# Kernel optimization log

Hardware: AMD Instinct MI355X
Metric: run time of the kernel (lower is better)

The kernel has to match this reference:

```python
import jax, jax.numpy as jnp
import numpy as np

N_NODES = 50000
N_FEAT = 63          # nodeChannels C = N_FEAT + 1 = 64
N_EDGES = 800000
N_LABELS = 10000
BATCH = 4
N_LAYERS = 5
C = N_FEAT + 1


def setup_inputs() -> dict:
    key = jax.random.key(0)
    ks = jax.random.split(key, 16)
    s = 0.05  # small init scale for numerical sanity
    return {
        "cov": jax.random.normal(ks[0], (BATCH, N_LABELS), jnp.float32),
        "nodes": jax.random.normal(ks[1], (N_NODES, N_FEAT), jnp.float32),
        "edges": jax.random.randint(ks[2], (2, N_EDGES), 0, N_NODES, jnp.int64 if jax.config.jax_enable_x64 else jnp.int32),
        "count2label": jnp.arange(N_LABELS, dtype=jnp.int32),
        "ggc_weight": jax.random.normal(ks[3], (N_LAYERS, C, C), jnp.float32) * s,
        "gru_w_ih": jax.random.normal(ks[4], (3 * C, C), jnp.float32) * s,
        "gru_w_hh": jax.random.normal(ks[5], (3 * C, C), jnp.float32) * s,
        "gru_b_ih": jax.random.normal(ks[6], (3 * C,), jnp.float32) * s,
        "gru_b_hh": jax.random.normal(ks[7], (3 * C,), jnp.float32) * s,
        "ai_w": jax.random.normal(ks[8], (2 * C, 2 * C), jnp.float32) * s,
        "ai_b": jax.random.normal(ks[9], (2 * C,), jnp.float32) * s,
        "aj_w": jax.random.normal(ks[10], (2 * C, 2 * C), jnp.float32) * s,
        "aj_b": jax.random.normal(ks[11], (2 * C,), jnp.float32) * s,
        "mlp_w": jax.random.normal(ks[12], (256, 2 * C), jnp.float32) * s,
        "mlp_b": jax.random.normal(ks[13], (256,), jnp.float32) * s,
        "critic_w": jax.random.normal(ks[14], (1, 256), jnp.float32) * s,
        "critic_b": jax.random.normal(ks[15], (1,), jnp.float32) * s,
    }


def _gru_cell(m, h, w_ih, w_hh, b_ih, b_hh):
    # torch GRUCell, gate order r, z, n
    gx = m @ w_ih.T + b_ih   # [..., 3C]
    gh = h @ w_hh.T + b_hh
    c = h.shape[-1]
    xr, xz, xn = gx[..., :c], gx[..., c:2 * c], gx[..., 2 * c:]
    hr, hz, hn = gh[..., :c], gh[..., c:2 * c], gh[..., 2 * c:]
    r = jax.nn.sigmoid(xr + hr)
    z = jax.nn.sigmoid(xz + hz)
    n = jnp.tanh(xn + r * hn)
    return (1.0 - z) * n + z * h


def reference(cov, nodes, edges, count2label, ggc_weight,
              gru_w_ih, gru_w_hh, gru_b_ih, gru_b_hh,
              ai_w, ai_b, aj_w, aj_b, mlp_w, mlp_b, critic_w, critic_b):
    n, f = nodes.shape
    b = cov.shape[0]
    # scatter coverage into per-graph node channel: covInGraph[count2label] = cov
    cov_in_graph = jnp.zeros((b, n), cov.dtype).at[:, count2label].set(cov)
    # batched node input [B, N, C]; batched graph = B identical copies w/ offset edges
    x0 = jnp.concatenate(
        [jnp.broadcast_to(nodes, (b, n, f)), cov_in_graph[..., None]], axis=-1)
    src, dst = edges[0], edges[1]

    def scatter_add(mb):  # [N, C] -> [N, C]: sum messages from source at target
        return jax.ops.segment_sum(mb[src], dst, num_segments=n)

    x = x0
    for i in range(ggc_weight.shape[0]):
        m = x @ ggc_weight[i]                     # dense per-layer matmul [B,N,C]
        agg = jax.vmap(scatter_add)(m)            # edge scatter-add propagate
        x = _gru_cell(agg, x, gru_w_ih, gru_w_hh, gru_b_ih, gru_b_hh)

    # attention gate: sigmoid(Wi cat) * relu(Wj cat), cat = [x, x0]
    cat = jnp.concatenate([x, x0], axis=-1)       # [B, N, 2C]
    att = jax.nn.sigmoid(cat @ ai_w.T + ai_b) * jax.nn.relu(cat @ aj_w.T + aj_b)
    pooled = jax.nn.relu(att.sum(axis=1))         # global_add_pool -> [B, 2C]
    state = jax.nn.relu(pooled @ mlp_w.T + mlp_b) # graphmlp
    return state @ critic_w.T + critic_b          # critic value [B, 1]
```

## Files before the change

kernel.cpp:

```cpp
#include <hip/hip_runtime.h>
#include <math.h>

#define NN 50000
#define NF 63
#define NE 800000
#define NL 10000
#define NB 4
#define NLAY 5
#define BN (NB*NN)
#define NTILES (BN/64)
#define SCAN_NBLK ((NN+255)/256)
#define HIST_NBLK ((NE+255)/256)

using f32x4  = __attribute__((ext_vector_type(4))) float;
using f32x2  = __attribute__((ext_vector_type(2))) float;
using bf16x8 = __attribute__((ext_vector_type(8))) __bf16;

__device__ __forceinline__ float frcp(float x){ return __builtin_amdgcn_rcpf(x); }
__device__ __forceinline__ float sigm(float v){ return frcp(1.f + __expf(-v)); }
__device__ __forceinline__ float tanh_f(float v){ return fmaf(-2.f, frcp(__expf(2.f*v) + 1.f), 1.f); }

__device__ __forceinline__ ushort f2bf(float f){
    uint u = __builtin_bit_cast(uint, f);
    u += 0x7fffu + ((u >> 16) & 1u);
    return (ushort)(u >> 16);
}
__device__ __forceinline__ float bf_lo(uint v){ return __builtin_bit_cast(float, v << 16); }
__device__ __forceinline__ float bfu(ushort v){ return __builtin_bit_cast(float, ((uint)v) << 16); }

__device__ __forceinline__ uchar f2fp8(float v){
    int enc = __builtin_amdgcn_cvt_pk_fp8_f32(v, v, 0, false);
    return (uchar)(enc & 0xff);
}

__device__ __forceinline__ bf16x8 ldfrag(const ushort* p){
    uint4 v = *(const uint4*)p;
    return __builtin_bit_cast(bf16x8, v);
}
__device__ __forceinline__ f32x4 MFMA(bf16x8 a, bf16x8 b, f32x4 c){
    return __builtin_amdgcn_mfma_f32_16x16x32_bf16(a, b, c, 0, 0, 0);
}

__global__ void k_setup(const int* __restrict__ edges, int* __restrict__ cnt,
                        const float* __restrict__ wih, const float* __restrict__ whh,
                        const float* __restrict__ aiw, const float* __restrict__ ajw,
                        const float* __restrict__ ggc,
                        ushort* __restrict__ whhb, ushort* __restrict__ aiwb,
                        ushort* __restrict__ ajwb, ushort* __restrict__ wfb){
    int bid = blockIdx.x;
    if (bid < HIST_NBLK){
        int e = bid*256 + threadIdx.x;
        if (e < NE) atomicAdd(&cnt[edges[NE + e]], 1);
        return;
    }
    int i = (bid - HIST_NBLK)*256 + threadIdx.x;
    if (i < 12288)        whhb[i]        = f2bf(whh[i]);
    else if (i < 28672)   aiwb[i-12288]  = f2bf(aiw[i-12288]);
    else if (i < 45056)   ajwb[i-28672]  = f2bf(ajw[i-28672]);
    else if (i < 106496){
        int t = i - 45056;
        int lay = t / 12288;
        int rem = t % 12288;
        int n = rem >> 6, k = rem & 63;
        const float* W  = ggc + lay*4096 + k*64;
        const float* wr = wih + n*64;
        float s = 0.f;
        #pragma unroll 8
        for (int c = 0; c < 64; ++c) s = fmaf(W[c], wr[c], s);
        wfb[t] = f2bf(s);
    }
}

__global__ void k_scan1(const int* __restrict__ cnt, int* __restrict__ tmp, int* __restrict__ bsum){
    __shared__ int sh[256];
    int tx = threadIdx.x, i = blockIdx.x*256 + tx;
    int v = (i < NN) ? cnt[i] : 0;
    sh[tx] = v; __syncthreads();
    for (int off = 1; off < 256; off <<= 1){
        int u = (tx >= off) ? sh[tx-off] : 0;
        __syncthreads();
        sh[tx] += u;
        __syncthreads();
    }
    int incl = sh[tx];
    if (i < NN) tmp[i] = incl - v;
    if (tx == 255) bsum[blockIdx.x] = incl;
}

__global__ void k_scan2(const int* __restrict__ bsum, int* __restrict__ boff){
    __shared__ int sh[256];
    int tx = threadIdx.x;
    int v = (tx < SCAN_NBLK) ? bsum[tx] : 0;
    sh[tx] = v; __syncthreads();
    for (int off = 1; off < 256; off <<= 1){
        int u = (tx >= off) ? sh[tx-off] : 0;
        __syncthreads();
        sh[tx] += u;
        __syncthreads();
    }
    boff[tx] = sh[tx] - v;
}

__global__ void k_scan3(const int* __restrict__ tmp, const int* __restrict__ boff,
                        int* __restrict__ row_start, int* __restrict__ cursor){
    int i = blockIdx.x*256 + threadIdx.x;
    if (i < NN){
        int rs = tmp[i] + boff[blockIdx.x];
        row_start[i] = rs;
        cursor[i] = rs;
    }
    if (i == 0) row_start[NN] = NE;
}

__global__ void k_fillcsr(const int* __restrict__ edges, int* __restrict__ cursor, int* __restrict__ csr_src){
    int e = blockIdx.x*256 + threadIdx.x;
    if (e < NE){
        int d = edges[NE + e];
        int pos = atomicAdd(&cursor[d], 1);
        csr_src[pos] = edges[e];
    }
}

__global__ void k_x0(const float* __restrict__ nodes, ushort* __restrict__ x0I,
                     uchar* __restrict__ x0F){
    int f = blockIdx.x*256 + threadIdx.x;
    int row = f >> 4, c4 = f & 15;
    int n = row % NN, b = row / NN;
    float v[4];
    #pragma unroll
    for (int i = 0; i < 4; ++i){
        int c = c4*4 + i;
        v[i] = (c < NF) ? nodes[(size_t)n*NF + c] : 0.f;
    }
    uint2 pk;
    pk.x = (uint)f2bf(v[0]) | ((uint)f2bf(v[1]) << 16);
    pk.y = (uint)f2bf(v[2]) | ((uint)f2bf(v[3]) << 16);
    *(uint2*)(x0I + ((size_t)n*4 + b)*64 + c4*4) = pk;
    if (b == 0){
        uint q = 0;
        q = (uint)__builtin_amdgcn_cvt_pk_fp8_f32(v[0], v[1], (int)q, false);
        q = (uint)__builtin_amdgcn_cvt_pk_fp8_f32(v[2], v[3], (int)q, true);
        *(uint*)(x0F + (size_t)n*64 + c4*4) = q;
    }
}

__global__ void k_cov(const float* __restrict__ cov, const int* __restrict__ c2l,
                      ushort* __restrict__ x0I, ushort* __restrict__ covB){
    int i = blockIdx.x*256 + threadIdx.x;
    if (i < NB*NL){
        int b = i / NL, j = i % NL;
        int nd = c2l[j];
        ushort vb = f2bf(cov[i]);
        x0I[((size_t)nd*4 + b)*64 + 63] = vb;
        covB[(size_t)nd*4 + b] = vb;
    }
}

template<bool LI>
__device__ __forceinline__ void gather0q(const uchar* __restrict__ x0F,
                                         const ushort* __restrict__ covB,
                                         const int* __restrict__ row_start,
                                         const int* __restrict__ csr_src,
                                         const int* sIdx, int estart,
                                         int d0, int l, ushort* __restrict__ sAgg,
                                         int rbase){
    const int qn = l >> 4, t = l & 15;
    const uint off = (uint)(t*4);
    const int d = d0 + qn;
    const int e0 = row_start[d], e1 = row_start[d+1];
    f32x2 a01 = (f32x2){0.f,0.f}, a23 = (f32x2){0.f,0.f};
    float c = 0.f;
    int e = e0;
    for (; e + 8 <= e1; e += 8){
        int s[8];
        #pragma unroll
        for (int j = 0; j < 8; ++j) s[j] = LI ? sIdx[e + j - estart] : csr_src[e + j];
        uint v[8];
        #pragma unroll
        for (int j = 0; j < 8; ++j) v[j] = *(const uint*)(x0F + (size_t)s[j]*64 + off);
        #pragma unroll
        for (int j = 0; j < 8; ++j){
            a01 += __builtin_amdgcn_cvt_pk_f32_fp8(v[j], false);
            a23 += __builtin_amdgcn_cvt_pk_f32_fp8(v[j], true);
        }
        if (t < 4){
            #pragma unroll
            for (int j = 0; j < 8; ++j) c += bf_lo((uint)covB[(size_t)s[j]*4 + t]);
        }
    }
    if (e < e1){
        #pragma unroll
        for (int j = 0; j < 8; ++j){
            int ee = e + j; bool ok = ee < e1; if (!ok) ee = e1 - 1;
            int s = LI ? sIdx[ee - estart] : csr_src[ee];
            uint v = *(const uint*)(x0F + (size_t)s*64 + off);
            if (!ok) v = 0u;
            a01 += __builtin_amdgcn_cvt_pk_f32_fp8(v, false);
            a23 += __builtin_amdgcn_cvt_pk_f32_fp8(v, true);
            if (t < 4){
                float cv = bf_lo((uint)covB[(size_t)s*4 + t]);
                c += ok ? cv : 0.f;
            }
        }
    }
    uint2 pk;
    pk.x = (uint)f2bf(a01.x) | ((uint)f2bf(a01.y) << 16);
    pk.y = (uint)f2bf(a23.x) | ((uint)f2bf(a23.y) << 16);
    #pragma unroll
    for (int b = 0; b < 4; ++b){
        float cb = __shfl(c, (l & 48) | b);
        uint2 o = pk;
        if (t == 15) o.y = (o.y & 0xffffu) | ((uint)f2bf(cb) << 16);
        *(uint2*)(&sAgg[(size_t)(rbase + qn*4 + b)*72 + t*4]) = o;
    }
}

template<bool LI>
__device__ __forceinline__ void gather4q(const uchar* __restrict__ xF,
                                         const int* __restrict__ row_start,
                                         const int* __restrict__ csr_src,
                                         const int* sIdx, int estart,
                                         int d0, int l, ushort* __restrict__ sAgg,
                                         int rbase){
    const int qn = l >> 4;
    const int t  = l & 15;
    const uint off = (uint)(t*16);
    const int d = d0 + qn;
    const int e0 = row_start[d], e1 = row_start[d+1];
    f32x2 ac[8];
    #pragma unroll
    for (int k = 0; k < 8; ++k) ac[k] = (f32x2){0.f,0.f};

    int e = e0;
    for (; e + 8 <= e1; e += 8){
        int s[8];
        #pragma unroll
        for (int j = 0; j < 8; ++j) s[j] = LI ? sIdx[e + j - estart] : csr_src[e + j];
        uint4 v[8];
        #pragma unroll
        for (int j = 0; j < 8; ++j) v[j] = *(const uint4*)(xF + (size_t)s[j]*256 + off);
        #pragma unroll
        for (int j = 0; j < 8; ++j){
            ac[0] += __builtin_amdgcn_cvt_pk_f32_fp8(v[j].x, false);
            ac[1] += __builtin_amdgcn_cvt_pk_f32_fp8(v[j].x, true);
            ac[2] += __builtin_amdgcn_cvt_pk_f32_fp8(v[j].y, false);
            ac[3] += __builtin_amdgcn_cvt_pk_f32_fp8(v[j].y, true);
            ac[4] += __builtin_amdgcn_cvt_pk_f32_fp8(v[j].z, false);
            ac[5] += __builtin_amdgcn_cvt_pk_f32_fp8(v[j].z, true);
            ac[6] += __builtin_amdgcn_cvt_pk_f32_fp8(v[j].w, false);
            ac[7] += __builtin_amdgcn_cvt_pk_f32_fp8(v[j].w, true);
        }
    }
    if (e < e1){
        #pragma unroll
        for (int j = 0; j < 8; ++j){
            int ee = e + j; bool ok = ee < e1; if (!ok) ee = e1 - 1;
            int s = LI ? sIdx[ee - estart] : csr_src[ee];
            uint4 v = *(const uint4*)(xF + (size_t)s*256 + off);
            if (!ok) v = (uint4){0u,0u,0u,0u};
            ac[0] += __builtin_amdgcn_cvt_pk_f32_fp8(v.x, false);
            ac[1] += __builtin_amdgcn_cvt_pk_f32_fp8(v.x, true);
            ac[2] += __builtin_amdgcn_cvt_pk_f32_fp8(v.y, false);
            ac[3] += __builtin_amdgcn_cvt_pk_f32_fp8(v.y, true);
            ac[4] += __builtin_amdgcn_cvt_pk_f32_fp8(v.z, false);
            ac[5] += __builtin_amdgcn_cvt_pk_f32_fp8(v.z, true);
            ac[6] += __builtin_amdgcn_cvt_pk_f32_fp8(v.w, false);
            ac[7] += __builtin_amdgcn_cvt_pk_f32_fp8(v.w, true);
        }
    }

    const int row = rbase + qn*4 + (t >> 2);
    const int c0  = (t & 3)*16;
    uint4 o0, o1;
    o0.x = (uint)f2bf(ac[0].x) | ((uint)f2bf(ac[0].y) << 16);
    o0.y = (uint)f2bf(ac[1].x) | ((uint)f2bf(ac[1].y) << 16);
    o0.z = (uint)f2bf(ac[2].x) | ((uint)f2bf(ac[2].y) << 16);
    o0.w = (uint)f2bf(ac[3].x) | ((uint)f2bf(ac[3].y) << 16);
    o1.x = (uint)f2bf(ac[4].x) | ((uint)f2bf(ac[4].y) << 16);
    o1.y = (uint)f2bf(ac[5].x) | ((uint)f2bf(ac[5].y) << 16);
    o1.z = (uint)f2bf(ac[6].x) | ((uint)f2bf(ac[6].y) << 16);
    o1.w = (uint)f2bf(ac[7].x) | ((uint)f2bf(ac[7].y) << 16);
    *(uint4*)(&sAgg[(size_t)row*72 + c0])     = o0;
    *(uint4*)(&sAgg[(size_t)row*72 + c0 + 8]) = o1;
}

__device__ __forceinline__ void gru_core(const ushort* sAgg, const ushort* sX,
                                         const ushort* __restrict__ wfb, const ushort* __restrict__ whhb,
                                         const float* __restrict__ bih, const float* __restrict__ bhh,
                                         int li, int q, int n0, float xv[4][4]){
    f32x4 Cr[4], Cz[4], Cxn[4], Chn[4];
    #pragma unroll
    for (int m = 0; m < 4; ++m){
        Cr[m]=(f32x4){0.f,0.f,0.f,0.f}; Cz[m]=(f32x4){0.f,0.f,0.f,0.f};
        Cxn[m]=(f32x4){0.f,0.f,0.f,0.f}; Chn[m]=(f32x4){0.f,0.f,0.f,0.f};
    }
    __builtin_amdgcn_s_setprio(1);
    #pragma unroll
    for (int ks = 0; ks < 4; ++ks){
        const ushort* wb = (ks < 2) ? wfb : whhb;
        const ushort* sT = (ks < 2) ? sAgg : sX;
        const int kb = (ks & 1)*32;
        bf16x8 Br = ldfrag(wb + (size_t)(n0 + li)*64 + kb + q*8);
        bf16x8 Bz = ldfrag(wb + (size_t)(64 + n0 + li)*64 + kb + q*8);
        bf16x8 Bn = ldfrag(wb + (size_t)(128 + n0 + li)*64 + kb + q*8);
        #pragma unroll
        for (int m = 0; m < 4; ++m){
            bf16x8 A = ldfrag(&sT[(m*16 + li)*72 + kb + q*8]);
            Cr[m] = MFMA(A, Br, Cr[m]);
            Cz[m] = MFMA(A, Bz, Cz[m]);
            if (ks < 2) Cxn[m] = MFMA(A, Bn, Cxn[m]);
            else        Chn[m] = MFMA(A, Bn, Chn[m]);
        }
    }
    __builtin_amdgcn_s_setprio(0);
    const int c = n0 + li;
    const float br_ = bih[c]     + bhh[c];
    const float bz_ = bih[64+c]  + bhh[64+c];
    const float bn_ = bih[128+c];
    const float bh_ = bhh[128+c];
    #pragma unroll
    for (int m = 0; m < 4; ++m){
        #pragma unroll
        for (int rg = 0; rg < 4; ++rg){
            int rl = m*16 + q*4 + rg;
            float r = sigm(Cr[m][rg] + br_);
            float z = sigm(Cz[m][rg] + bz_);
            float nng = tanh_f(Cxn[m][rg] + bn_ + r*(Chn[m][rg] + bh_));
            xv[m][rg] = (1.f - z)*nng + z*bfu(sX[rl*72 + c]);
        }
    }
}

__global__ __launch_bounds__(256) void k_gru0f(const uchar* __restrict__ x0F,
                                               const ushort* __restrict__ covB,
                                               const int* __restrict__ row_start,
                                               const int* __restrict__ csr_src,
                                               const ushort* __restrict__ x0I,
                                               const ushort* __restrict__ wfb, const ushort* __restrict__ whhb,
                                               const float* __restrict__ bih, const float* __restrict__ bhh,
                                               ushort* __restrict__ xout, uchar* __restrict__ xFout){
    __shared__ __align__(16) ushort sAgg[64*72];
    __shared__ __align__(16) ushort sX[64*72];
    __shared__ int sIdx[1024];
    const int tx = threadIdx.x;
    const int l  = tx & 63, li = l & 15, q = l >> 4;
    const int w  = __builtin_amdgcn_readfirstlane(tx >> 6);
    const int R0 = blockIdx.x*64;
    const int n0 = blockIdx.x*16;
    const int estart = row_start[n0], eend = row_start[n0 + 16];
    const int ecnt = eend - estart;

    #pragma unroll
    for (int it = 0; it < 2; ++it){
        int idx = it*256 + tx, r = idx >> 3, g = idx & 7;
        *(uint4*)(&sX[r*72 + g*8]) = *(const uint4*)(x0I + (size_t)(R0 + r)*64 + g*8);
    }
    for (int k = tx; k < ecnt && k < 1024; k += 256) sIdx[k] = csr_src[estart + k];
    __syncthreads();

    if (ecnt <= 1024) gather0q<true >(x0F, covB, row_start, csr_src, sIdx, estart, n0 + w*4, l, sAgg, w*16);
    else              gather0q<false>(x0F, covB, row_start, csr_src, sIdx, estart, n0 + w*4, l, sAgg, w*16);
    __syncthreads();

    float xv[4][4];
    gru_core(sAgg, sX, wfb, whhb, bih, bhh, li, q, 16*w, xv);

    const int c = 16*w + li;
    #pragma unroll
    for (int m = 0; m < 4; ++m)
        #pragma unroll
        for (int rg = 0; rg < 4; ++rg){
            size_t ro = (size_t)(R0 + m*16 + q*4 + rg)*64 + c;
            xout[ro]  = f2bf(xv[m][rg]);
            xFout[ro] = f2fp8(xv[m][rg]);
        }
}

__global__ __launch_bounds__(256) void k_gruFf(const uchar* __restrict__ xFin,
                                               const int* __restrict__ row_start,
                                               const int* __restrict__ csr_src,
                                               const ushort* __restrict__ xsrc,
                                               const ushort* __restrict__ wfb, const ushort* __restrict__ whhb,
                                               const float* __restrict__ bih, const float* __restrict__ bhh,
                                               ushort* __restrict__ xout, uchar* __restrict__ xFout){
    __shared__ __align__(16) ushort sAgg[64*72];
    __shared__ __align__(16) ushort sX[64*72];
    __shared__ int sIdx[1024];
    const int tx = threadIdx.x;
    const int l  = tx & 63, li = l & 15, q = l >> 4;
    const int w  = __builtin_amdgcn_readfirstlane(tx >> 6);
    const int R0 = blockIdx.x*64;
    const int n0 = blockIdx.x*16;
    const int estart = row_start[n0], eend = row_start[n0 + 16];
    const int ecnt = eend - estart;

    #pragma unroll
    for (int it = 0; it < 2; ++it){
        int idx = it*256 + tx, r = idx >> 3, g = idx & 7;
        *(uint4*)(&sX[r*72 + g*8]) = *(const uint4*)(xsrc + (size_t)(R0 + r)*64 + g*8);
    }
    for (int k = tx; k < ecnt && k < 1024; k += 256) sIdx[k] = csr_src[estart + k];
    __syncthreads();

    if (ecnt <= 1024) gather4q<true >(xFin, row_start, csr_src, sIdx, estart, n0 + w*4, l, sAgg, w*16);
    else              gather4q<false>(xFin, row_start, csr_src, sIdx, estart, n0 + w*4, l, sAgg, w*16);
    __syncthreads();

    float xv[4][4];
    gru_core(sAgg, sX, wfb, whhb, bih, bhh, li, q, 16*w, xv);

    const int c = 16*w + li;
    #pragma unroll
    for (int m = 0; m < 4; ++m)
        #pragma unroll
        for (int rg = 0; rg < 4; ++rg){
            size_t ro = (size_t)(R0 + m*16 + q*4 + rg)*64 + c;
            xout[ro]  = f2bf(xv[m][rg]);
            xFout[ro] = f2fp8(xv[m][rg]);
        }
}

__global__ __launch_bounds__(256) void k_gruLf(const uchar* __restrict__ xFin,
                                               const int* __restrict__ row_start,
                                               const int* __restrict__ csr_src,
                                               const ushort* __restrict__ xsrc,
                                               const ushort* __restrict__ wfb, const ushort* __restrict__ whhb,
                                               const float* __restrict__ bih, const float* __restrict__ bhh,
                                               const ushort* __restrict__ x0I,
                                               const ushort* __restrict__ aiwb, const float* __restrict__ aib,
                                               const ushort* __restrict__ ajwb, const float* __restrict__ ajb,
                                               float* __restrict__ pooled16){
    __shared__ __align__(16) ushort sAgg[64*72];
    __shared__ __align__(16) ushort sX[64*72];
    __shared__ int sIdx[1024];
    const int tx = threadIdx.x;
    const int l  = tx & 63, li = l & 15, q = l >> 4;
    const int w  = __builtin_amdgcn_readfirstlane(tx >> 6);
    const int R0 = blockIdx.x*64;
    const int n0 = blockIdx.x*16;
    const int estart = row_start[n0], eend = row_start[n0 + 16];
    const int ecnt = eend - estart;

    #pragma unroll
    for (int it = 0; it < 2; ++it){
        int idx = it*256 + tx, r = idx >> 3, g = idx & 7;
        *(uint4*)(&sX[r*72 + g*8]) = *(const uint4*)(xsrc + (size_t)(R0 + r)*64 + g*8);
    }
    for (int k = tx; k < ecnt && k < 1024; k += 256) sIdx[k] = csr_src[estart + k];
    __syncthreads();

    if (ecnt <= 1024) gather4q<true >(xFin, row_start, csr_src, sIdx, estart, n0 + w*4, l, sAgg, w*16);
    else              gather4q<false>(xFin, row_start, csr_src, sIdx, estart, n0 + w*4, l, sAgg, w*16);
    __syncthreads();

    float xv[4][4];
    gru_core(sAgg, sX, wfb, whhb, bih, bhh, li, q, 16*w, xv);
    __syncthreads();

    const int c = 16*w + li;
    #pragma unroll
    for (int m = 0; m < 4; ++m)
        #pragma unroll
        for (int rg = 0; rg < 4; ++rg)
            sAgg[(m*16 + q*4 + rg)*72 + c] = f2bf(xv[m][rg]);
    #pragma unroll
    for (int it = 0; it < 2; ++it){
        int idx = it*256 + tx, r = idx >> 3, g = idx & 7;
        *(uint4*)(&sX[r*72 + g*8]) = *(const uint4*)(x0I + (size_t)(R0 + r)*64 + g*8);
    }
    __syncthreads();

    f32x4 Ai[2][4], Aj[2][4];
    #pragma unroll
    for (int t = 0; t < 2; ++t)
        #pragma unroll
        for (int m = 0; m < 4; ++m){ Ai[t][m]=(f32x4){0.f,0.f,0.f,0.f}; Aj[t][m]=(f32x4){0.f,0.f,0.f,0.f}; }

    const int nb0 = 32*w;
    __builtin_amdgcn_s_setprio(1);
    #pragma unroll
    for (int ks = 0; ks < 4; ++ks){
        const ushort* sT = (ks < 2) ? sAgg : sX;
        const int kb = (ks & 1)*32;
        bf16x8 Bi[2], Bj[2];
        #pragma unroll
        for (int t = 0; t < 2; ++t){
            Bi[t] = ldfrag(aiwb + (size_t)(nb0 + 16*t + li)*128 + ks*32 + q*8);
            Bj[t] = ldfrag(ajwb + (size_t)(nb0 + 16*t + li)*128 + ks*32 + q*8);
        }
        #pragma unroll
        for (int m = 0; m < 4; ++m){
            bf16x8 A = ldfrag(&sT[(m*16 + li)*72 + kb + q*8]);
            #pragma unroll
            for (int t = 0; t < 2; ++t){
                Ai[t][m] = MFMA(A, Bi[t], Ai[t][m]);
                Aj[t][m] = MFMA(A, Bj[t], Aj[t][m]);
            }
        }
    }
    __builtin_amdgcn_s_setprio(0);

    float* pb = pooled16 + (size_t)(blockIdx.x & 15)*512;
    #pragma unroll
    for (int t = 0; t < 2; ++t){
        int cc = nb0 + 16*t + li;
        float bia = aib[cc], bja = ajb[cc];
        float vs[4] = {0.f, 0.f, 0.f, 0.f};
        #pragma unroll
        for (int m = 0; m < 4; ++m){
            #pragma unroll
            for (int rg = 0; rg < 4; ++rg){
                float s = sigm(Ai[t][m][rg] + bia);
                float a = Aj[t][m][rg] + bja;
                a = a > 0.f ? a : 0.f;
                vs[rg] += s*a;
            }
        }
        #pragma unroll
        for (int b = 0; b < 4; ++b){
            vs[b] += __shfl_xor(vs[b], 16);
            vs[b] += __shfl_xor(vs[b], 32);
        }
        if (l < 16){
            #pragma unroll
            for (int b = 0; b < 4; ++b) atomicAdd(&pb[b*128 + nb0 + 16*t + l], vs[b]);
        }
    }
}

__global__ void k_final(const float* __restrict__ pooled16, const float* __restrict__ mw,
                        const float* __restrict__ mb, const float* __restrict__ cw,
                        const float* __restrict__ cb, float* __restrict__ out){
    __shared__ float red[256];
    int t = threadIdx.x;
    int b = blockIdx.x;
    float acc = mb[t];
    #pragma unroll 4
    for (int k = 0; k < 128; ++k){
        float p = 0.f;
        #pragma unroll
        for (int kb = 0; kb < 16; ++kb) p += pooled16[kb*512 + b*128 + k];
        p = p > 0.f ? p : 0.f;
        acc = fmaf(p, mw[t*128 + k], acc);
    }
    float st = acc > 0.f ? acc : 0.f;
    red[t] = st * cw[t];
    __syncthreads();
    for (int off = 128; off > 0; off >>= 1){
        if (t < off) red[t] += red[t + off];
        __syncthreads();
    }
    if (t == 0) out[b] = red[0] + cb[0];
}

extern "C" void kernel_launch(void* const* d_in, const int* in_sizes, int n_in,
                              void* d_out, int out_size, void* d_ws, size_t ws_size,
                              hipStream_t stream) {
    const float* cov   = (const float*)d_in[0];
    const float* nodes = (const float*)d_in[1];
    const int*   edges = (const int*)d_in[2];
    const int*   c2l   = (const int*)d_in[3];
    const float* ggc   = (const float*)d_in[4];
    const float* wih   = (const float*)d_in[5];
    const float* whh   = (const float*)d_in[6];
    const float* bih   = (const float*)d_in[7];
    const float* bhh   = (const float*)d_in[8];
    const float* aiw   = (const float*)d_in[9];
    const float* aib   = (const float*)d_in[10];
    const float* ajw   = (const float*)d_in[11];
    const float* ajb   = (const float*)d_in[12];
    const float* mlpw  = (const float*)d_in[13];
    const float* mlpb  = (const float*)d_in[14];
    const float* cw    = (const float*)d_in[15];
    const float* cb    = (const float*)d_in[16];
    float* out = (float*)d_out;

    const size_t XSZ = (size_t)BN * 64;
    float* ws = (float*)d_ws;
    float* pooled16 = ws;
    ushort* xS    = (ushort*)(pooled16 + 8192);
    ushort* x0I   = xS + XSZ;
    ushort* aggx  = x0I + XSZ;
    ushort* covB  = aggx + XSZ;
    ushort* whhb  = covB + (size_t)NN*4;
    ushort* aiwb  = whhb + 12288;
    ushort* ajwb  = aiwb + 16384;
    ushort* wfb   = ajwb + 16384;
    uchar* xF     = (uchar*)(wfb + 61440);
    uchar* x0F    = xF + XSZ;
    int* cnt       = (int*)(x0F + (size_t)NN*64);
    int* tmp       = cnt + NN;
    int* bsum      = tmp + NN;
    int* boff      = bsum + 256;
    int* row_start = boff + 256;
    int* cursor    = row_start + (NN + 1);
    int* csr_src   = cursor + NN;

    hipMemsetAsync(cnt, 0, (size_t)NN*sizeof(int), stream);
    hipMemsetAsync(pooled16, 0, 8192*sizeof(float), stream);
    hipMemsetAsync(covB, 0, (size_t)NN*4*sizeof(ushort), stream);

    k_setup<<<HIST_NBLK + 416, 256, 0, stream>>>(edges, cnt, wih, whh, aiw, ajw, ggc,
                                                 whhb, aiwb, ajwb, wfb);
    k_scan1<<<SCAN_NBLK, 256, 0, stream>>>(cnt, tmp, bsum);
    k_scan2<<<1, 256, 0, stream>>>(bsum, boff);
    k_scan3<<<SCAN_NBLK, 256, 0, stream>>>(tmp, boff, row_start, cursor);
    k_fillcsr<<<(NE + 255)/256, 256, 0, stream>>>(edges, cursor, csr_src);

    k_x0<<<(BN*16)/256, 256, 0, stream>>>(nodes, x0I, x0F);
    k_cov<<<(NB*NL + 255)/256, 256, 0, stream>>>(cov, c2l, x0I, covB);

    uchar* xFbuf[2] = { xF, (uchar*)aggx };

    for (int i = 0; i < NLAY; ++i){
        const ushort* wf = wfb + (size_t)i*12288;
        if (i == 0){
            k_gru0f<<<NTILES, 256, 0, stream>>>(x0F, covB, row_start, csr_src, x0I,
                                                wf, whhb, bih, bhh, xS, xFbuf[0]);
        } else if (i < NLAY - 1){
            k_gruFf<<<NTILES, 256, 0, stream>>>(xFbuf[(i+1)&1], row_start, csr_src, xS,
                                                wf, whhb, bih, bhh, xS, xFbuf[i&1]);
        } else {
            k_gruLf<<<NTILES, 256, 0, stream>>>(xFbuf[(i+1)&1], row_start, csr_src, xS,
                                                wf, whhb, bih, bhh,
                                                x0I, aiwb, aib, ajwb, ajb, pooled16);
        }
    }

    k_final<<<NB, 256, 0, stream>>>(pooled16, mlpw, mlpb, cw, cb, out);
    (void)in_sizes; (void)n_in; (void)out_size; (void)ws_size;
}
```

Measured before the change: 568.8 us.

## Fuse setup kernels, drop LDS index staging, unroll gathers, coalesce state stores

Folds the x0 conversion into the setup launch and the coverage scatter into the first scan launch, which removes two kernel launches. Removes the shared-memory staging of CSR indices so the gathers read csr_src directly, and raises the gather unroll from 8 to 16 for more loads in flight. GRU output is now staged through LDS and written as coalesced 16-byte bf16 and fp8 stores instead of scattered scalar stores. Launch bounds request 4 blocks per CU; the wider unroll raises register pressure.

Measured after the change: 490.1 us. -13.8%, faster.

```diff
diff --git a/kernel.cpp b/kernel.cpp
--- a/kernel.cpp
+++ b/kernel.cpp
@@ -11,6 +11,8 @@
 #define NTILES (BN/64)
 #define SCAN_NBLK ((NN+255)/256)
 #define HIST_NBLK ((NE+255)/256)
+#define X0_NBLK ((BN*16)/256)
+#define COV_NBLK ((NB*NL+255)/256)
 
 using f32x4  = __attribute__((ext_vector_type(4))) float;
 using f32x2  = __attribute__((ext_vector_type(2))) float;
@@ -26,12 +28,8 @@
     return (ushort)(u >> 16);
 }
 __device__ __forceinline__ float bf_lo(uint v){ return __builtin_bit_cast(float, v << 16); }
+__device__ __forceinline__ float bf_hi(uint v){ return __builtin_bit_cast(float, v & 0xffff0000u); }
 __device__ __forceinline__ float bfu(ushort v){ return __builtin_bit_cast(float, ((uint)v) << 16); }
-
-__device__ __forceinline__ uchar f2fp8(float v){
-    int enc = __builtin_amdgcn_cvt_pk_fp8_f32(v, v, 0, false);
-    return (uchar)(enc & 0xff);
-}
 
 __device__ __forceinline__ bf16x8 ldfrag(const ushort* p){
     uint4 v = *(const uint4*)p;
@@ -46,32 +44,69 @@
                         const float* __restrict__ aiw, const float* __restrict__ ajw,
                         const float* __restrict__ ggc,
                         ushort* __restrict__ whhb, ushort* __restrict__ aiwb,
-                        ushort* __restrict__ ajwb, ushort* __restrict__ wfb){
+                        ushort* __restrict__ ajwb, ushort* __restrict__ wfb,
+                        const float* __restrict__ nodes, ushort* __restrict__ x0I,
+                        uchar* __restrict__ x0F){
     int bid = blockIdx.x;
     if (bid < HIST_NBLK){
         int e = bid*256 + threadIdx.x;
         if (e < NE) atomicAdd(&cnt[edges[NE + e]], 1);
         return;
     }
-    int i = (bid - HIST_NBLK)*256 + threadIdx.x;
-    if (i < 12288)        whhb[i]        = f2bf(whh[i]);
-    else if (i < 28672)   aiwb[i-12288]  = f2bf(aiw[i-12288]);
-    else if (i < 45056)   ajwb[i-28672]  = f2bf(ajw[i-28672]);
-    else if (i < 106496){
-        int t = i - 45056;
-        int lay = t / 12288;
-        int rem = t % 12288;
-        int n = rem >> 6, k = rem & 63;
-        const float* W  = ggc + lay*4096 + k*64;
-        const float* wr = wih + n*64;
-        float s = 0.f;
-        #pragma unroll 8
-        for (int c = 0; c < 64; ++c) s = fmaf(W[c], wr[c], s);
-        wfb[t] = f2bf(s);
-    }
-}
-
-__global__ void k_scan1(const int* __restrict__ cnt, int* __restrict__ tmp, int* __restrict__ bsum){
+    if (bid < HIST_NBLK + 416){
+        int i = (bid - HIST_NBLK)*256 + threadIdx.x;
+        if (i < 12288)        whhb[i]        = f2bf(whh[i]);
+        else if (i < 28672)   aiwb[i-12288]  = f2bf(aiw[i-12288]);
+        else if (i < 45056)   ajwb[i-28672]  = f2bf(ajw[i-28672]);
+        else if (i < 106496){
+            int t = i - 45056;
+            int lay = t / 12288;
+            int rem = t % 12288;
+            int n = rem >> 6, k = rem & 63;
+            const float* W  = ggc + lay*4096 + k*64;
+            const float* wr = wih + n*64;
+            float s = 0.f;
+            #pragma unroll 8
+            for (int c = 0; c < 64; ++c) s = fmaf(W[c], wr[c], s);
+            wfb[t] = f2bf(s);
+        }
+        return;
+    }
+    int f = (bid - HIST_NBLK - 416)*256 + threadIdx.x;
+    int row = f >> 4, c4 = f & 15;
+    int n = row % NN, b = row / NN;
+    float v[4];
+    #pragma unroll
+    for (int i = 0; i < 4; ++i){
+        int c = c4*4 + i;
+        v[i] = (c < NF) ? nodes[(size_t)n*NF + c] : 0.f;
+    }
+    uint2 pk;
+    pk.x = (uint)f2bf(v[0]) | ((uint)f2bf(v[1]) << 16);
+    pk.y = (uint)f2bf(v[2]) | ((uint)f2bf(v[3]) << 16);
+    *(uint2*)(x0I + ((size_t)n*4 + b)*64 + c4*4) = pk;
+    if (b == 0){
+        uint q = 0;
+        q = (uint)__builtin_amdgcn_cvt_pk_fp8_f32(v[0], v[1], (int)q, false);
+        q = (uint)__builtin_amdgcn_cvt_pk_fp8_f32(v[2], v[3], (int)q, true);
+        *(uint*)(x0F + (size_t)n*64 + c4*4) = q;
+    }
+}
+
+__global__ void k_scan1(const int* __restrict__ cnt, int* __restrict__ tmp, int* __restrict__ bsum,
+                        const float* __restrict__ cov, const int* __restrict__ c2l,
+                        ushort* __restrict__ x0I, ushort* __restrict__ covB){
+    if (blockIdx.x >= SCAN_NBLK){
+        int i = (blockIdx.x - SCAN_NBLK)*256 + threadIdx.x;
+        if (i < NB*NL){
+            int b = i / NL, j = i % NL;
+            int nd = c2l[j];
+            ushort vb = f2bf(cov[i]);
+            x0I[((size_t)nd*4 + b)*64 + 63] = vb;
+            covB[(size_t)nd*4 + b] = vb;
+        }
+        return;
+    }
     __shared__ int sh[256];
     int tx = threadIdx.x, i = blockIdx.x*256 + tx;
     int v = (i < NN) ? cnt[i] : 0;
@@ -121,47 +156,10 @@
     }
 }
 
-__global__ void k_x0(const float* __restrict__ nodes, ushort* __restrict__ x0I,
-                     uchar* __restrict__ x0F){
-    int f = blockIdx.x*256 + threadIdx.x;
-    int row = f >> 4, c4 = f & 15;
-    int n = row % NN, b = row / NN;
-    float v[4];
-    #pragma unroll
-    for (int i = 0; i < 4; ++i){
-        int c = c4*4 + i;
-        v[i] = (c < NF) ? nodes[(size_t)n*NF + c] : 0.f;
-    }
-    uint2 pk;
-    pk.x = (uint)f2bf(v[0]) | ((uint)f2bf(v[1]) << 16);
-    pk.y = (uint)f2bf(v[2]) | ((uint)f2bf(v[3]) << 16);
-    *(uint2*)(x0I + ((size_t)n*4 + b)*64 + c4*4) = pk;
-    if (b == 0){
-        uint q = 0;
-        q = (uint)__builtin_amdgcn_cvt_pk_fp8_f32(v[0], v[1], (int)q, false);
-        q = (uint)__builtin_amdgcn_cvt_pk_fp8_f32(v[2], v[3], (int)q, true);
-        *(uint*)(x0F + (size_t)n*64 + c4*4) = q;
-    }
-}
-
-__global__ void k_cov(const float* __restrict__ cov, const int* __restrict__ c2l,
-                      ushort* __restrict__ x0I, ushort* __restrict__ covB){
-    int i = blockIdx.x*256 + threadIdx.x;
-    if (i < NB*NL){
-        int b = i / NL, j = i % NL;
-        int nd = c2l[j];
-        ushort vb = f2bf(cov[i]);
-        x0I[((size_t)nd*4 + b)*64 + 63] = vb;
-        covB[(size_t)nd*4 + b] = vb;
-    }
-}
-
-template<bool LI>
 __device__ __forceinline__ void gather0q(const uchar* __restrict__ x0F,
                                          const ushort* __restrict__ covB,
                                          const int* __restrict__ row_start,
                                          const int* __restrict__ csr_src,
-                                         const int* sIdx, int estart,
                                          int d0, int l, ushort* __restrict__ sAgg,
                                          int rbase){
     const int qn = l >> 4, t = l & 15;
@@ -171,35 +169,43 @@
     f32x2 a01 = (f32x2){0.f,0.f}, a23 = (f32x2){0.f,0.f};
     float c = 0.f;
     int e = e0;
-    for (; e + 8 <= e1; e += 8){
-        int s[8];
-        #pragma unroll
-        for (int j = 0; j < 8; ++j) s[j] = LI ? sIdx[e + j - estart] : csr_src[e + j];
-        uint v[8];
-        #pragma unroll
-        for (int j = 0; j < 8; ++j) v[j] = *(const uint*)(x0F + (size_t)s[j]*64 + off);
-        #pragma unroll
-        for (int j = 0; j < 8; ++j){
+    for (; e + 16 <= e1; e += 16){
+        int s[16];
+        #pragma unroll
+        for (int j = 0; j < 16; ++j) s[j] = csr_src[e + j];
+        uint v[16];
+        #pragma unroll
+        for (int j = 0; j < 16; ++j) v[j] = *(const uint*)(x0F + (size_t)s[j]*64 + off);
+        #pragma unroll
+        for (int j = 0; j < 16; ++j){
             a01 += __builtin_amdgcn_cvt_pk_f32_fp8(v[j], false);
             a23 += __builtin_amdgcn_cvt_pk_f32_fp8(v[j], true);
         }
         if (t < 4){
             #pragma unroll
-            for (int j = 0; j < 8; ++j) c += bf_lo((uint)covB[(size_t)s[j]*4 + t]);
+            for (int j = 0; j < 16; ++j) c += bf_lo((uint)covB[(size_t)s[j]*4 + t]);
         }
     }
     if (e < e1){
-        #pragma unroll
-        for (int j = 0; j < 8; ++j){
-            int ee = e + j; bool ok = ee < e1; if (!ok) ee = e1 - 1;
-            int s = LI ? sIdx[ee - estart] : csr_src[ee];
-            uint v = *(const uint*)(x0F + (size_t)s*64 + off);
-            if (!ok) v = 0u;
-            a01 += __builtin_amdgcn_cvt_pk_f32_fp8(v, false);
-            a23 += __builtin_amdgcn_cvt_pk_f32_fp8(v, true);
-            if (t < 4){
-                float cv = bf_lo((uint)covB[(size_t)s*4 + t]);
-                c += ok ? cv : 0.f;
+        int s[16];
+        #pragma unroll
+        for (int j = 0; j < 16; ++j){ int ee = e + j; if (ee >= e1) ee = e1 - 1; s[j] = csr_src[ee]; }
+        uint v[16];
+        #pragma unroll
+        for (int j = 0; j < 16; ++j){
+            v[j] = *(const uint*)(x0F + (size_t)s[j]*64 + off);
+            if (e + j >= e1) v[j] = 0u;
+        }
+        #pragma unroll
+        for (int j = 0; j < 16; ++j){
+            a01 += __builtin_amdgcn_cvt_pk_f32_fp8(v[j], false);
+            a23 += __builtin_amdgcn_cvt_pk_f32_fp8(v[j], true);
+        }
+        if (t < 4){
+            #pragma unroll
+            for (int j = 0; j < 16; ++j){
+                float cv = bf_lo((uint)covB[(size_t)s[j]*4 + t]);
+                c += (e + j < e1) ? cv : 0.f;
             }
         }
     }
@@ -215,11 +221,9 @@
     }
 }
 
-template<bool LI>
 __device__ __forceinline__ void gather4q(const uchar* __restrict__ xF,
                                          const int* __restrict__ row_start,
                                          const int* __restrict__ csr_src,
-                                         const int* sIdx, int estart,
                                          int d0, int l, ushort* __restrict__ sAgg,
                                          int rbase){
     const int qn = l >> 4;
@@ -232,15 +236,15 @@
     for (int k = 0; k < 8; ++k) ac[k] = (f32x2){0.f,0.f};
 
     int e = e0;
-    for (; e + 8 <= e1; e += 8){
-        int s[8];
-        #pragma unroll
-        for (int j = 0; j < 8; ++j) s[j] = LI ? sIdx[e + j - estart] : csr_src[e + j];
-        uint4 v[8];
-        #pragma unroll
-        for (int j = 0; j < 8; ++j) v[j] = *(const uint4*)(xF + (size_t)s[j]*256 + off);
-        #pragma unroll
-        for (int j = 0; j < 8; ++j){
+    for (; e + 16 <= e1; e += 16){
+        int s[16];
+        #pragma unroll
+        for (int j = 0; j < 16; ++j) s[j] = csr_src[e + j];
+        uint4 v[16];
+        #pragma unroll
+        for (int j = 0; j < 16; ++j) v[j] = *(const uint4*)(xF + (size_t)s[j]*256 + off);
+        #pragma unroll
+        for (int j = 0; j < 16; ++j){
             ac[0] += __builtin_amdgcn_cvt_pk_f32_fp8(v[j].x, false);
             ac[1] += __builtin_amdgcn_cvt_pk_f32_fp8(v[j].x, true);
             ac[2] += __builtin_amdgcn_cvt_pk_f32_fp8(v[j].y, false);
@@ -252,20 +256,25 @@
         }
     }
     if (e < e1){
-        #pragma unroll
-        for (int j = 0; j < 8; ++j){
-            int ee = e + j; bool ok = ee < e1; if (!ok) ee = e1 - 1;
-            int s = LI ? sIdx[ee - estart] : csr_src[ee];
-            uint4 v = *(const uint4*)(xF + (size_t)s*256 + off);
-            if (!ok) v = (uint4){0u,0u,0u,0u};
-            ac[0] += __builtin_amdgcn_cvt_pk_f32_fp8(v.x, false);
-            ac[1] += __builtin_amdgcn_cvt_pk_f32_fp8(v.x, true);
-            ac[2] += __builtin_amdgcn_cvt_pk_f32_fp8(v.y, false);
-            ac[3] += __builtin_amdgcn_cvt_pk_f32_fp8(v.y, true);
-            ac[4] += __builtin_amdgcn_cvt_pk_f32_fp8(v.z, false);
-            ac[5] += __builtin_amdgcn_cvt_pk_f32_fp8(v.z, true);
-            ac[6] += __builtin_amdgcn_cvt_pk_f32_fp8(v.w, false);
-            ac[7] += __builtin_amdgcn_cvt_pk_f32_fp8(v.w, true);
+        int s[16];
+        #pragma unroll
+        for (int j = 0; j < 16; ++j){ int ee = e + j; if (ee >= e1) ee = e1 - 1; s[j] = csr_src[ee]; }
+        uint4 v[16];
+        #pragma unroll
+        for (int j = 0; j < 16; ++j){
+            v[j] = *(const uint4*)(xF + (size_t)s[j]*256 + off);
+            if (e + j >= e1) v[j] = (uint4){0u,0u,0u,0u};
+        }
+        #pragma unroll
+        for (int j = 0; j < 16; ++j){
+            ac[0] += __builtin_amdgcn_cvt_pk_f32_fp8(v[j].x, false);
+            ac[1] += __builtin_amdgcn_cvt_pk_f32_fp8(v[j].x, true);
+            ac[2] += __builtin_amdgcn_cvt_pk_f32_fp8(v[j].y, false);
+            ac[3] += __builtin_amdgcn_cvt_pk_f32_fp8(v[j].y, true);
+            ac[4] += __builtin_amdgcn_cvt_pk_f32_fp8(v[j].z, false);
+            ac[5] += __builtin_amdgcn_cvt_pk_f32_fp8(v[j].z, true);
+            ac[6] += __builtin_amdgcn_cvt_pk_f32_fp8(v[j].w, false);
+            ac[7] += __builtin_amdgcn_cvt_pk_f32_fp8(v[j].w, true);
         }
     }
 
@@ -331,7 +340,45 @@
     }
 }
 
-__global__ __launch_bounds__(256) void k_gru0f(const uchar* __restrict__ x0F,
+__device__ __forceinline__ void store_state(ushort* sAgg, int tx, int w, int li, int q,
+                                            const float xv[4][4], int R0,
+                                            ushort* __restrict__ xout, uchar* __restrict__ xFout){
+    __syncthreads();
+    const int c = 16*w + li;
+    #pragma unroll
+    for (int m = 0; m < 4; ++m)
+        #pragma unroll
+        for (int rg = 0; rg < 4; ++rg)
+            sAgg[(m*16 + q*4 + rg)*72 + c] = f2bf(xv[m][rg]);
+    __syncthreads();
+    #pragma unroll
+    for (int it = 0; it < 2; ++it){
+        int idx = it*256 + tx, r = idx >> 3, g = idx & 7;
+        *(uint4*)(xout + (size_t)(R0 + r)*64 + g*8) = *(const uint4*)(&sAgg[r*72 + g*8]);
+    }
+    {
+        int r = tx >> 2, g = tx & 3;
+        const ushort* src = &sAgg[r*72 + g*16];
+        uint4 a = *(const uint4*)src;
+        uint4 b = *(const uint4*)(src + 8);
+        uint4 o; uint qd;
+        qd = (uint)__builtin_amdgcn_cvt_pk_fp8_f32(bf_lo(a.x), bf_hi(a.x), 0, false);
+        qd = (uint)__builtin_amdgcn_cvt_pk_fp8_f32(bf_lo(a.y), bf_hi(a.y), (int)qd, true);
+        o.x = qd;
+        qd = (uint)__builtin_amdgcn_cvt_pk_fp8_f32(bf_lo(a.z), bf_hi(a.z), 0, false);
+        qd = (uint)__builtin_amdgcn_cvt_pk_fp8_f32(bf_lo(a.w), bf_hi(a.w), (int)qd, true);
+        o.y = qd;
+        qd = (uint)__builtin_amdgcn_cvt_pk_fp8_f32(bf_lo(b.x), bf_hi(b.x), 0, false);
+        qd = (uint)__builtin_amdgcn_cvt_pk_fp8_f32(bf_lo(b.y), bf_hi(b.y), (int)qd, true);
+        o.z = qd;
+        qd = (uint)__builtin_amdgcn_cvt_pk_fp8_f32(bf_lo(b.z), bf_hi(b.z), 0, false);
+        qd = (uint)__builtin_amdgcn_cvt_pk_fp8_f32(bf_lo(b.w), bf_hi(b.w), (int)qd, true);
+        o.w = qd;
+        *(uint4*)(xFout + (size_t)(R0 + r)*64 + g*16) = o;
+    }
+}
+
+__global__ __launch_bounds__(256, 4) void k_gru0f(const uchar* __restrict__ x0F,
                                                const ushort* __restrict__ covB,
                                                const int* __restrict__ row_start,
                                                const int* __restrict__ csr_src,
@@ -341,42 +388,25 @@
                                                ushort* __restrict__ xout, uchar* __restrict__ xFout){
     __shared__ __align__(16) ushort sAgg[64*72];
     __shared__ __align__(16) ushort sX[64*72];
-    __shared__ int sIdx[1024];
     const int tx = threadIdx.x;
     const int l  = tx & 63, li = l & 15, q = l >> 4;
     const int w  = __builtin_amdgcn_readfirstlane(tx >> 6);
     const int R0 = blockIdx.x*64;
-    const int n0 = blockIdx.x*16;
-    const int estart = row_start[n0], eend = row_start[n0 + 16];
-    const int ecnt = eend - estart;
 
     #pragma unroll
     for (int it = 0; it < 2; ++it){
         int idx = it*256 + tx, r = idx >> 3, g = idx & 7;
         *(uint4*)(&sX[r*72 + g*8]) = *(const uint4*)(x0I + (size_t)(R0 + r)*64 + g*8);
     }
-    for (int k = tx; k < ecnt && k < 1024; k += 256) sIdx[k] = csr_src[estart + k];
-    __syncthreads();
-
-    if (ecnt <= 1024) gather0q<true >(x0F, covB, row_start, csr_src, sIdx, estart, n0 + w*4, l, sAgg, w*16);
-    else              gather0q<false>(x0F, covB, row_start, csr_src, sIdx, estart, n0 + w*4, l, sAgg, w*16);
+    gather0q(x0F, covB, row_start, csr_src, blockIdx.x*16 + w*4, l, sAgg, w*16);
     __syncthreads();
 
     float xv[4][4];
     gru_core(sAgg, sX, wfb, whhb, bih, bhh, li, q, 16*w, xv);
-
-    const int c = 16*w + li;
-    #pragma unroll
-    for (int m = 0; m < 4; ++m)
-        #pragma unroll
-        for (int rg = 0; rg < 4; ++rg){
-            size_t ro = (size_t)(R0 + m*16 + q*4 + rg)*64 + c;
-            xout[ro]  = f2bf(xv[m][rg]);
-            xFout[ro] = f2fp8(xv[m][rg]);
-        }
-}
-
-__global__ __launch_bounds__(256) void k_gruFf(const uchar* __restrict__ xFin,
+    store_state(sAgg, tx, w, li, q, xv, R0, xout, xFout);
+}
+
+__global__ __launch_bounds__(256, 4) void k_gruFf(const uchar* __restrict__ xFin,
                                                const int* __restrict__ row_start,
                                                const int* __restrict__ csr_src,
                                                const ushort* __restrict__ xsrc,
@@ -385,42 +415,25 @@
                                                ushort* __restrict__ xout, uchar* __restrict__ xFout){
     __shared__ __align__(16) ushort sAgg[64*72];
     __shared__ __align__(16) ushort sX[64*72];
-    __shared__ int sIdx[1024];
     const int tx = threadIdx.x;
     const int l  = tx & 63, li = l & 15, q = l >> 4;
     const int w  = __builtin_amdgcn_readfirstlane(tx >> 6);
     const int R0 = blockIdx.x*64;
-    const int n0 = blockIdx.x*16;
-    const int estart = row_start[n0], eend = row_start[n0 + 16];
-    const int ecnt = eend - estart;
 
     #pragma unroll
     for (int it = 0; it < 2; ++it){
         int idx = it*256 + tx, r = idx >> 3, g = idx & 7;
         *(uint4*)(&sX[r*72 + g*8]) = *(const uint4*)(xsrc + (size_t)(R0 + r)*64 + g*8);
     }
-    for (int k = tx; k < ecnt && k < 1024; k += 256) sIdx[k] = csr_src[estart + k];
-    __syncthreads();
-
-    if (ecnt <= 1024) gather4q<true >(xFin, row_start, csr_src, sIdx, estart, n0 + w*4, l, sAgg, w*16);
-    else              gather4q<false>(xFin, row_start, csr_src, sIdx, estart, n0 + w*4, l, sAgg, w*16);
+    gather4q(xFin, row_start, csr_src, blockIdx.x*16 + w*4, l, sAgg, w*16);
     __syncthreads();
 
     float xv[4][4];
     gru_core(sAgg, sX, wfb, whhb, bih, bhh, li, q, 16*w, xv);
-
-    const int c = 16*w + li;
-    #pragma unroll
-    for (int m = 0; m < 4; ++m)
-        #pragma unroll
-        for (int rg = 0; rg < 4; ++rg){
-            size_t ro = (size_t)(R0 + m*16 + q*4 + rg)*64 + c;
-            xout[ro]  = f2bf(xv[m][rg]);
-            xFout[ro] = f2fp8(xv[m][rg]);
-        }
-}
-
-__global__ __launch_bounds__(256) void k_gruLf(const uchar* __restrict__ xFin,
+    store_state(sAgg, tx, w, li, q, xv, R0, xout, xFout);
+}
+
+__global__ __launch_bounds__(256, 4) void k_gruLf(const uchar* __restrict__ xFin,
                                                const int* __restrict__ row_start,
                                                const int* __restrict__ csr_src,
                                                const ushort* __restrict__ xsrc,
@@ -432,25 +445,17 @@
                                                float* __restrict__ pooled16){
     __shared__ __align__(16) ushort sAgg[64*72];
     __shared__ __align__(16) ushort sX[64*72];
-    __shared__ int sIdx[1024];
     const int tx = threadIdx.x;
     const int l  = tx & 63, li = l & 15, q = l >> 4;
     const int w  = __builtin_amdgcn_readfirstlane(tx >> 6);
     const int R0 = blockIdx.x*64;
-    const int n0 = blockIdx.x*16;
-    const int estart = row_start[n0], eend = row_start[n0 + 16];
-    const int ecnt = eend - estart;
 
     #pragma unroll
     for (int it = 0; it < 2; ++it){
         int idx = it*256 + tx, r = idx >> 3, g = idx & 7;
         *(uint4*)(&sX[r*72 + g*8]) = *(const uint4*)(xsrc + (size_t)(R0 + r)*64 + g*8);
     }
-    for (int k = tx; k < ecnt && k < 1024; k += 256) sIdx[k] = csr_src[estart + k];
-    __syncthreads();
-
-    if (ecnt <= 1024) gather4q<true >(xFin, row_start, csr_src, sIdx, estart, n0 + w*4, l, sAgg, w*16);
-    else              gather4q<false>(xFin, row_start, csr_src, sIdx, estart, n0 + w*4, l, sAgg, w*16);
+    gather4q(xFin, row_start, csr_src, blockIdx.x*16 + w*4, l, sAgg, w*16);
     __syncthreads();
 
     float xv[4][4];
@@ -600,15 +605,13 @@
     hipMemsetAsync(pooled16, 0, 8192*sizeof(float), stream);
     hipMemsetAsync(covB, 0, (size_t)NN*4*sizeof(ushort), stream);
 
-    k_setup<<<HIST_NBLK + 416, 256, 0, stream>>>(edges, cnt, wih, whh, aiw, ajw, ggc,
-                                                 whhb, aiwb, ajwb, wfb);
-    k_scan1<<<SCAN_NBLK, 256, 0, stream>>>(cnt, tmp, bsum);
+    k_setup<<<HIST_NBLK + 416 + X0_NBLK, 256, 0, stream>>>(edges, cnt, wih, whh, aiw, ajw, ggc,
+                                                           whhb, aiwb, ajwb, wfb,
+                                                           nodes, x0I, x0F);
+    k_scan1<<<SCAN_NBLK + COV_NBLK, 256, 0, stream>>>(cnt, tmp, bsum, cov, c2l, x0I, covB);
     k_scan2<<<1, 256, 0, stream>>>(bsum, boff);
     k_scan3<<<SCAN_NBLK, 256, 0, stream>>>(tmp, boff, row_start, cursor);
     k_fillcsr<<<(NE + 255)/256, 256, 0, stream>>>(edges, cursor, csr_src);
-
-    k_x0<<<(BN*16)/256, 256, 0, stream>>>(nodes, x0I, x0F);
-    k_cov<<<(NB*NL + 255)/256, 256, 0, stream>>>(cov, c2l, x0I, covB);
 
     uchar* xFbuf[2] = { xF, (uchar*)aggx };
 
```
